# Optimization experiments

Measured on AMD Instinct MI355X. Metric: run time of the kernel, lower is better.

The kernel has to match this reference:

```python
import jax, jax.numpy as jnp
import numpy as np

N_NODES = 100000
N_EDGES = 1600000
N_FEAT = 128
N_HID = 128
N_CLS = 40
DROP_P = 0.5


def setup_inputs() -> dict:
    key = jax.random.key(0)
    k1, k2, k3, k4 = jax.random.split(key, 4)
    x = jax.random.normal(k1, (N_NODES, N_FEAT), dtype=jnp.float32)
    edge_index = jax.random.randint(k2, (2, N_EDGES), 0, N_NODES, dtype=jnp.int32)
    W1 = jax.random.normal(k3, (N_FEAT, N_HID), dtype=jnp.float32) / np.sqrt(N_FEAT)
    b1 = jnp.zeros((N_HID,), dtype=jnp.float32)
    W2 = jax.random.normal(k4, (N_HID, N_CLS), dtype=jnp.float32) / np.sqrt(N_HID)
    b2 = jnp.zeros((N_CLS,), dtype=jnp.float32)
    return {"x": x, "edge_index": edge_index, "W1": W1, "b1": b1, "W2": W2, "b2": b2}


def _gcn_norm(edge_index, num_nodes):
    # add self-loops, then symmetric normalization D^-1/2 (A+I) D^-1/2
    loops = jnp.arange(num_nodes, dtype=edge_index.dtype)
    src = jnp.concatenate([edge_index[0], loops])
    dst = jnp.concatenate([edge_index[1], loops])
    deg = jax.ops.segment_sum(jnp.ones_like(dst, dtype=jnp.float32), dst,
                              num_segments=num_nodes)
    deg_isqrt = jax.lax.rsqrt(deg)  # deg >= 1 thanks to self-loops
    norm = deg_isqrt[src] * deg_isqrt[dst]  # [E+N]
    return src, dst, norm


def _gcn_conv(x, src, dst, norm, W, b, num_nodes):
    h = x @ W                                   # [N, out]
    msg = h[src] * norm[:, None]                # gather + scale, [E+N, out]
    out = jax.ops.segment_sum(msg, dst, num_segments=num_nodes)  # scatter-add
    return out + b


def reference(x, edge_index, W1, b1, W2, b2):
    num_nodes = x.shape[0]
    src, dst, norm = _gcn_norm(edge_index, num_nodes)
    h = _gcn_conv(x, src, dst, norm, W1, b1, num_nodes)
    h = jax.nn.relu(h)
    # dropout(p=0.5, training=True) with a fixed key for determinism
    keep = jax.random.uniform(jax.random.key(42), h.shape) >= DROP_P
    h = jnp.where(keep, h / (1.0 - DROP_P), 0.0)
    out = _gcn_conv(h, src, dst, norm, W2, b2, num_nodes)
    return out
```

## Files before the change

kernel.cpp:

```cpp
#include <hip/hip_runtime.h>

#define N_NODES 100000
#define N_EDGES 1600000
#define NBUCK 196
#define G1B 3125
#define BCAP 9216

__device__ __forceinline__ unsigned pack_bf16(float a, float b){
  unsigned ua = __float_as_uint(a), ub = __float_as_uint(b);
  ua = ua + 0x7fffu + ((ua >> 16) & 1u);
  ub = ub + 0x7fffu + ((ub >> 16) & 1u);
  return (ua >> 16) | (ub & 0xffff0000u);
}
__device__ __forceinline__ unsigned short bf16_of(float a){
  unsigned ua = __float_as_uint(a);
  ua = ua + 0x7fffu + ((ua >> 16) & 1u);
  return (unsigned short)(ua >> 16);
}
__device__ __forceinline__ float bf_lo(unsigned u){ return __uint_as_float(u << 16); }
__device__ __forceinline__ float bf_hi(unsigned u){ return __uint_as_float(u & 0xffff0000u); }

__device__ __forceinline__ unsigned tf_rotl(unsigned x, int r){ return (x<<r)|(x>>(32-r)); }

__device__ __forceinline__ unsigned dropout_keep(unsigned e){
  unsigned x0 = 0u, x1 = e;
  const unsigned k0 = 0u, k1v = 42u;
  const unsigned k2 = 0x1BD11BDAu ^ k0 ^ k1v;
#define TF_R(r) { x0 += x1; x1 = tf_rotl(x1,(r)); x1 ^= x0; }
  x0 += k0; x1 += k1v;
  TF_R(13) TF_R(15) TF_R(26) TF_R(6)
  x0 += k1v; x1 += k2 + 1u;
  TF_R(17) TF_R(29) TF_R(16) TF_R(24)
  x0 += k2; x1 += k0 + 2u;
  TF_R(13) TF_R(15) TF_R(26) TF_R(6)
  x0 += k0; x1 += k1v + 3u;
  TF_R(17) TF_R(29) TF_R(16) TF_R(24)
  x0 += k1v; x1 += k2 + 4u;
  TF_R(13) TF_R(15) TF_R(26) TF_R(6)
  x0 += k2; x1 += k0 + 5u;
#undef TF_R
  return (x0 ^ x1) >> 31;
}

__device__ __forceinline__ void gemm1_block(int gb, int t, float* smem,
                                            const float* __restrict__ x,
                                            const float* __restrict__ W1,
                                            unsigned* __restrict__ h1g){
  float* xs = smem;
  float* Wq = smem + 4096;
  size_t row0 = (size_t)gb * 32;

  const float4* xv = (const float4*)(x + row0*128);
  float4* xsv = (float4*)xs;
  #pragma unroll
  for (int j = 0; j < 4; j++) xsv[t + 256*j] = xv[t + 256*j];

  int tx = t & 31, ty = t >> 5;
  float acc[4][4] = {};
  const float4* Wv = (const float4*)W1;
  float4* Wqv = (float4*)Wq;
  const float* xr = xs + (ty*4)*128;

  for (int q = 0; q < 4; q++){
    __syncthreads();
    #pragma unroll
    for (int j = 0; j < 4; j++) Wqv[t + 256*j] = Wv[q*1024 + t + 256*j];
    __syncthreads();
    int kbase = q*32;
    #pragma unroll 8
    for (int kk = 0; kk < 32; kk++){
      float4 w = *(const float4*)(Wq + kk*128 + tx*4);
      int k = kbase + kk;
      float x0 = xr[k], x1 = xr[128 + k], x2 = xr[256 + k], x3 = xr[384 + k];
      acc[0][0] = fmaf(x0, w.x, acc[0][0]); acc[0][1] = fmaf(x0, w.y, acc[0][1]);
      acc[0][2] = fmaf(x0, w.z, acc[0][2]); acc[0][3] = fmaf(x0, w.w, acc[0][3]);
      acc[1][0] = fmaf(x1, w.x, acc[1][0]); acc[1][1] = fmaf(x1, w.y, acc[1][1]);
      acc[1][2] = fmaf(x1, w.z, acc[1][2]); acc[1][3] = fmaf(x1, w.w, acc[1][3]);
      acc[2][0] = fmaf(x2, w.x, acc[2][0]); acc[2][1] = fmaf(x2, w.y, acc[2][1]);
      acc[2][2] = fmaf(x2, w.z, acc[2][2]); acc[2][3] = fmaf(x2, w.w, acc[2][3]);
      acc[3][0] = fmaf(x3, w.x, acc[3][0]); acc[3][1] = fmaf(x3, w.y, acc[3][1]);
      acc[3][2] = fmaf(x3, w.z, acc[3][2]); acc[3][3] = fmaf(x3, w.w, acc[3][3]);
    }
  }
  #pragma unroll
  for (int i = 0; i < 4; i++){
    uint2 o;
    o.x = pack_bf16(acc[i][0], acc[i][1]);
    o.y = pack_bf16(acc[i][2], acc[i][3]);
    *(uint2*)(h1g + (row0 + ty*4 + i)*64 + tx*2) = o;
  }
}

__launch_bounds__(256)
__global__ void k_B(const float* __restrict__ x, const float* __restrict__ W1,
                    unsigned* __restrict__ h1g,
                    const int* __restrict__ src, const int* __restrict__ dst,
                    int* __restrict__ bcur2,
                    int* __restrict__ tmpS, int* __restrict__ tmpD, int N, int E){
  extern __shared__ float smem[];
  int t = threadIdx.x;
  if (blockIdx.x < NBUCK){
    int* hist = (int*)smem;
    int fb = blockIdx.x;
    for (int i = t; i < NBUCK; i += 256) hist[i] = 0;
    __syncthreads();
    int e0 = fb*8192;
    #pragma unroll 4
    for (int j = 0; j < 32; j++){
      int e = e0 + t + j*256;
      if (e < E) atomicAdd(&hist[dst[e] >> 9], 1);
    }
    __syncthreads();
    if (t < NBUCK){
      int c = hist[t];
      if (c > 0) hist[t] = t*BCAP + atomicAdd(&bcur2[t], c);
    }
    __syncthreads();
    #pragma unroll 4
    for (int j = 0; j < 32; j++){
      int e = e0 + t + j*256;
      if (e < E){
        int d = dst[e], s = src[e];
        int p = atomicAdd(&hist[d >> 9], 1);
        tmpS[p] = s;
        tmpD[p] = d;
      }
    }
    return;
  }
  int gb = blockIdx.x - NBUCK;
  if (gb < G1B) gemm1_block(gb, t, smem, x, W1, h1g);
}

__launch_bounds__(512)
__global__ void k_hist(const int* __restrict__ tmpD, const int* __restrict__ bcur2,
                       int* __restrict__ degi, int* __restrict__ off,
                       float* __restrict__ dii, int N){
  __shared__ int cur[512];
  __shared__ int wtot[8];
  int b = blockIdx.x, t = threadIdx.x;
  cur[t] = 0;
  __syncthreads();
  int m = bcur2[b];
  int base = b*BCAP;
  int node0 = b << 9;
  for (int i = t; i < m; i += 512)
    atomicAdd(&cur[tmpD[base + i] - node0], 1);
  __syncthreads();
  int v = cur[t];
  int lane = t & 63, w = t >> 6;
  int incl = v;
  for (int d = 1; d < 64; d <<= 1){
    int y = __shfl_up(incl, d);
    if (lane >= d) incl += y;
  }
  if (lane == 63) wtot[w] = incl;
  __syncthreads();
  int wb = 0;
  for (int i = 0; i < w; i++) wb += wtot[i];
  int excl = wb + incl - v;
  int n = node0 + t;
  if (n < N){
    degi[n] = v;
    off[n]  = base + excl;
    dii[n]  = rsqrtf((float)(v + 1));
  }
}

__launch_bounds__(1024)
__global__ void k_csort(const int* __restrict__ tmpS, const int* __restrict__ tmpD,
                        int2* __restrict__ csre, const int* __restrict__ off,
                        const int* __restrict__ bcur2, const float* __restrict__ dii,
                        int N){
  __shared__ int   cur[512];
  __shared__ float dl[512];
  int b = blockIdx.x, t = threadIdx.x;
  int node0 = b << 9;
  if (t < 512){
    int n = node0 + t;
    cur[t] = (n < N) ? off[n] : 0;
    dl[t]  = (n < N) ? dii[n] : 0.f;
  }
  __syncthreads();
  int m = bcur2[b];
  int base = b*BCAP;
  for (int i = t; i < m; i += 1024){
    int s = tmpS[base + i];
    int d = tmpD[base + i];
    int dloc = d - node0;
    float w = dii[s] * dl[dloc];
    int p = atomicAdd(&cur[dloc], 1);
    csre[p] = make_int2(s, __float_as_int(w));
  }
}

__launch_bounds__(256)
__global__ void k_agg1(const unsigned* __restrict__ h1g, unsigned* __restrict__ Bbg,
                       const int2* __restrict__ csre, const int* __restrict__ off,
                       const int* __restrict__ degi, const float* __restrict__ dii,
                       const float* __restrict__ b1, int N){
  int n = blockIdx.x*4 + (threadIdx.x >> 6);
  int lane = threadIdx.x & 63;
  if (n >= N) return;
  n = __builtin_amdgcn_readfirstlane(n);
  float din = dii[n];
  float s2 = din*din;
  unsigned su = h1g[(size_t)n*64 + lane];
  float a0 = bf_lo(su)*s2, a1 = bf_hi(su)*s2;
  int o = off[n], cnt = degi[n];
  int i = 0;
  for (; i + 8 <= cnt; i += 8){
    int2 e0 = csre[o+i+0], e1 = csre[o+i+1], e2 = csre[o+i+2], e3 = csre[o+i+3];
    int2 e4 = csre[o+i+4], e5 = csre[o+i+5], e6 = csre[o+i+6], e7 = csre[o+i+7];
    unsigned u0 = h1g[(size_t)e0.x*64 + lane];
    unsigned u1 = h1g[(size_t)e1.x*64 + lane];
    unsigned u2 = h1g[(size_t)e2.x*64 + lane];
    unsigned u3 = h1g[(size_t)e3.x*64 + lane];
    unsigned u4 = h1g[(size_t)e4.x*64 + lane];
    unsigned u5 = h1g[(size_t)e5.x*64 + lane];
    unsigned u6 = h1g[(size_t)e6.x*64 + lane];
    unsigned u7 = h1g[(size_t)e7.x*64 + lane];
    float w0 = __int_as_float(e0.y), w1 = __int_as_float(e1.y);
    float w2 = __int_as_float(e2.y), w3 = __int_as_float(e3.y);
    float w4 = __int_as_float(e4.y), w5 = __int_as_float(e5.y);
    float w6 = __int_as_float(e6.y), w7 = __int_as_float(e7.y);
    a0 = fmaf(bf_lo(u0), w0, a0); a1 = fmaf(bf_hi(u0), w0, a1);
    a0 = fmaf(bf_lo(u1), w1, a0); a1 = fmaf(bf_hi(u1), w1, a1);
    a0 = fmaf(bf_lo(u2), w2, a0); a1 = fmaf(bf_hi(u2), w2, a1);
    a0 = fmaf(bf_lo(u3), w3, a0); a1 = fmaf(bf_hi(u3), w3, a1);
    a0 = fmaf(bf_lo(u4), w4, a0); a1 = fmaf(bf_hi(u4), w4, a1);
    a0 = fmaf(bf_lo(u5), w5, a0); a1 = fmaf(bf_hi(u5), w5, a1);
    a0 = fmaf(bf_lo(u6), w6, a0); a1 = fmaf(bf_hi(u6), w6, a1);
    a0 = fmaf(bf_lo(u7), w7, a0); a1 = fmaf(bf_hi(u7), w7, a1);
  }
  for (; i < cnt; ++i){
    int2 e = csre[o+i];
    unsigned u = h1g[(size_t)e.x*64 + lane];
    float w = __int_as_float(e.y);
    a0 = fmaf(bf_lo(u), w, a0); a1 = fmaf(bf_hi(u), w, a1);
  }
  float2 bb = *(const float2*)(b1 + lane*2);
  a0 = fmaxf(a0 + bb.x, 0.f);
  a1 = fmaxf(a1 + bb.y, 0.f);
  unsigned e0i = (unsigned)n*128u + (unsigned)lane*2u;
  a0 = dropout_keep(e0i)      ? a0*2.f : 0.f;
  a1 = dropout_keep(e0i + 1u) ? a1*2.f : 0.f;
  Bbg[(size_t)n*64 + lane] = pack_bf16(a0, a1);
}

__launch_bounds__(256)
__global__ void k_gemm2(const unsigned* __restrict__ Bbg, const float* __restrict__ W2,
                        unsigned short* __restrict__ h2g, int N){
  __shared__ float W2T[40*132];
  __shared__ float Bs[64*132];
  int t = threadIdx.x;
  int row0 = blockIdx.x * 64;
  for (int idx = t; idx < 128*40; idx += 256){
    int r = idx / 40, c = idx - 40*r;
    W2T[c*132 + r] = W2[idx];
  }
  #pragma unroll
  for (int j = 0; j < 8; j++){
    int idx = t + 256*j;
    int r = idx >> 5, c2 = idx & 31;
    int gr = row0 + r; if (gr > N-1) gr = N-1;
    uint2 v = *(const uint2*)(Bbg + (size_t)gr*64 + c2*2);
    float4 f = { bf_lo(v.x), bf_hi(v.x), bf_lo(v.y), bf_hi(v.y) };
    *(float4*)(Bs + r*132 + c2*4) = f;
  }
  __syncthreads();

  int cg = t & 7, rg = t >> 3;
  int c0 = cg*5, r0 = rg*2;
  float acc[2][5] = {};
  #pragma unroll 4
  for (int k = 0; k < 128; k++){
    float bv0 = Bs[r0*132 + k], bv1 = Bs[(r0+1)*132 + k];
    #pragma unroll
    for (int u = 0; u < 5; u++){
      float w = W2T[(c0+u)*132 + k];
      acc[0][u] = fmaf(bv0, w, acc[0][u]);
      acc[1][u] = fmaf(bv1, w, acc[1][u]);
    }
  }
  #pragma unroll
  for (int i = 0; i < 2; i++){
    int gr = row0 + r0 + i;
    if (gr < N){
      #pragma unroll
      for (int u = 0; u < 5; u++) h2g[(size_t)gr*40 + c0 + u] = bf16_of(acc[i][u]);
    }
  }
}

__launch_bounds__(256)
__global__ void k_agg2(const unsigned* __restrict__ h2u, float* __restrict__ out,
                       const int2* __restrict__ csre, const int* __restrict__ off,
                       const int* __restrict__ degi, const float* __restrict__ dii,
                       const float* __restrict__ b2, int N){
  int n = blockIdx.x*4 + (threadIdx.x >> 6);
  int lane = threadIdx.x & 63;
  if (n >= N) return;
  n = __builtin_amdgcn_readfirstlane(n);
  int g = lane / 20;
  int c = lane - 20*g;
  bool act = g < 3;
  float din = dii[n];
  float a0 = 0.f, a1 = 0.f;
  if (g == 0){
    unsigned u = h2u[(size_t)n*20 + c];
    float s2 = din*din;
    float2 bb = *(const float2*)(b2 + 2*c);
    a0 = bf_lo(u)*s2 + bb.x;
    a1 = bf_hi(u)*s2 + bb.y;
  }
  int o = off[n], cnt = degi[n];
  int i = 0;
  for (; i + 6 <= cnt; i += 6){
    int2 ea = csre[o+i+0], eb = csre[o+i+1], ec = csre[o+i+2];
    int2 ed = csre[o+i+3], ee = csre[o+i+4], ef = csre[o+i+5];
    int   sA = (g==0) ? ea.x : (g==1) ? eb.x : ec.x;
    float wA = __int_as_float((g==0) ? ea.y : (g==1) ? eb.y : ec.y);
    int   sB = (g==0) ? ed.x : (g==1) ? ee.x : ef.x;
    float wB = __int_as_float((g==0) ? ed.y : (g==1) ? ee.y : ef.y);
    unsigned uA = 0u, uB = 0u;
    if (act){
      uA = h2u[(size_t)sA*20 + c];
      uB = h2u[(size_t)sB*20 + c];
    } else { wA = 0.f; wB = 0.f; }
    a0 = fmaf(bf_lo(uA), wA, a0); a1 = fmaf(bf_hi(uA), wA, a1);
    a0 = fmaf(bf_lo(uB), wB, a0); a1 = fmaf(bf_hi(uB), wB, a1);
  }
  for (; i + 3 <= cnt; i += 3){
    int2 ea = csre[o+i+0], eb = csre[o+i+1], ec = csre[o+i+2];
    int   s = (g==0) ? ea.x : (g==1) ? eb.x : ec.x;
    float w = __int_as_float((g==0) ? ea.y : (g==1) ? eb.y : ec.y);
    unsigned u = 0u;
    if (act) u = h2u[(size_t)s*20 + c];
    else w = 0.f;
    a0 = fmaf(bf_lo(u), w, a0); a1 = fmaf(bf_hi(u), w, a1);
  }
  for (; i < cnt; ++i){
    int2 e = csre[o+i];
    if (g == 0){
      unsigned u = h2u[(size_t)e.x*20 + c];
      float w = __int_as_float(e.y);
      a0 = fmaf(bf_lo(u), w, a0); a1 = fmaf(bf_hi(u), w, a1);
    }
  }
  float t0 = __shfl(a0, (lane+20) & 63), t1 = __shfl(a1, (lane+20) & 63);
  float u0 = __shfl(a0, (lane+40) & 63), u1 = __shfl(a1, (lane+40) & 63);
  if (g == 0){
    a0 += t0 + u0; a1 += t1 + u1;
    *(float2*)(out + (size_t)n*40 + c*2) = make_float2(a0, a1);
  }
}

extern "C" void kernel_launch(void* const* d_in, const int* in_sizes, int n_in,
                              void* d_out, int out_size, void* d_ws, size_t ws_size,
                              hipStream_t stream){
  const float* x  = (const float*)d_in[0];
  const int*   ei = (const int*)  d_in[1];
  const float* W1 = (const float*)d_in[2];
  const float* b1 = (const float*)d_in[3];
  const float* W2 = (const float*)d_in[4];
  const float* b2 = (const float*)d_in[5];
  float* out = (float*)d_out;
  char* ws = (char*)d_ws;
  const int N = N_NODES, E = N_EDGES;
  const int* srcv = ei;
  const int* dstv = ei + E;

  int*   bcur2 = (int*)  (ws + 0);
  int*   off   = (int*)  (ws + 8192);
  int*   degi  = (int*)  (ws + 417792);
  float* dii   = (float*)(ws + 827392);
  int*   tmpS  = (int*)  (ws + 1236992);
  int*   tmpD  = (int*)  (ws + 8462336);
  int2*  csre  = (int2*) (ws + 15687680);
  unsigned*       h1g = (unsigned*)      (ws + 30138368);
  unsigned short* h2g = (unsigned short*)(ws + 30138368);
  unsigned*       Bbg = (unsigned*)      (ws + 55738368);

  hipMemsetAsync(bcur2, 0, 1024, stream);

  k_B<<<NBUCK + G1B, 256, 32768, stream>>>(x, W1, h1g, srcv, dstv, bcur2, tmpS, tmpD, N, E);
  k_hist<<<NBUCK, 512, 0, stream>>>(tmpD, bcur2, degi, off, dii, N);
  k_csort<<<NBUCK, 1024, 0, stream>>>(tmpS, tmpD, csre, off, bcur2, dii, N);

  k_agg1 <<<N/4, 256, 0, stream>>>(h1g, Bbg, csre, off, degi, dii, b1, N);
  k_gemm2<<<(N + 63)/64, 256, 0, stream>>>(Bbg, W2, h2g, N);
  k_agg2 <<<N/4, 256, 0, stream>>>((const unsigned*)h2g, out, csre, off, degi, dii, b2, N);
}
```

Baseline: 239.4 us.

## Pad layer-2 features to 128-byte rows and pack the bucket temporaries

k_gemm2 now writes h2 with a 64-element row stride, so each row is a 128-byte-aligned line. k_agg2 is rewritten so that each 32-lane half reads one padded row per edge, with an 8-way unrolled gather in place of the 3-group split and the cross-lane shuffle reduction. The bucket-fill stage packs src/dst into a single int2 temporary and uses more, smaller edge chunks (4096 edges per block). The aim is to cut partial-line gathers and lane-selection overhead in aggregation, at the cost of more bytes per gathered row and redundant work in the upper half-wave.

```diff
diff --git a/kernel.cpp b/kernel.cpp
--- a/kernel.cpp
+++ b/kernel.cpp
@@ -4,6 +4,8 @@
 #define N_EDGES 1600000
 #define NBUCK 196
 #define G1B 3125
+#define FB 391
+#define FEDGE 4096
 #define BCAP 9216
 
 __device__ __forceinline__ unsigned pack_bf16(float a, float b){
@@ -95,18 +97,17 @@
 __global__ void k_B(const float* __restrict__ x, const float* __restrict__ W1,
                     unsigned* __restrict__ h1g,
                     const int* __restrict__ src, const int* __restrict__ dst,
-                    int* __restrict__ bcur2,
-                    int* __restrict__ tmpS, int* __restrict__ tmpD, int N, int E){
+                    int* __restrict__ bcur2, int2* __restrict__ tmp, int N, int E){
   extern __shared__ float smem[];
   int t = threadIdx.x;
-  if (blockIdx.x < NBUCK){
+  if (blockIdx.x < FB){
     int* hist = (int*)smem;
     int fb = blockIdx.x;
     for (int i = t; i < NBUCK; i += 256) hist[i] = 0;
     __syncthreads();
-    int e0 = fb*8192;
+    int e0 = fb*FEDGE;
     #pragma unroll 4
-    for (int j = 0; j < 32; j++){
+    for (int j = 0; j < FEDGE/256; j++){
       int e = e0 + t + j*256;
       if (e < E) atomicAdd(&hist[dst[e] >> 9], 1);
     }
@@ -117,23 +118,22 @@
     }
     __syncthreads();
     #pragma unroll 4
-    for (int j = 0; j < 32; j++){
+    for (int j = 0; j < FEDGE/256; j++){
       int e = e0 + t + j*256;
       if (e < E){
         int d = dst[e], s = src[e];
         int p = atomicAdd(&hist[d >> 9], 1);
-        tmpS[p] = s;
-        tmpD[p] = d;
+        tmp[p] = make_int2(s, d);
       }
     }
     return;
   }
-  int gb = blockIdx.x - NBUCK;
+  int gb = blockIdx.x - FB;
   if (gb < G1B) gemm1_block(gb, t, smem, x, W1, h1g);
 }
 
 __launch_bounds__(512)
-__global__ void k_hist(const int* __restrict__ tmpD, const int* __restrict__ bcur2,
+__global__ void k_hist(const int2* __restrict__ tmp, const int* __restrict__ bcur2,
                        int* __restrict__ degi, int* __restrict__ off,
                        float* __restrict__ dii, int N){
   __shared__ int cur[512];
@@ -145,7 +145,7 @@
   int base = b*BCAP;
   int node0 = b << 9;
   for (int i = t; i < m; i += 512)
-    atomicAdd(&cur[tmpD[base + i] - node0], 1);
+    atomicAdd(&cur[tmp[base + i].y - node0], 1);
   __syncthreads();
   int v = cur[t];
   int lane = t & 63, w = t >> 6;
@@ -168,10 +168,9 @@
 }
 
 __launch_bounds__(1024)
-__global__ void k_csort(const int* __restrict__ tmpS, const int* __restrict__ tmpD,
-                        int2* __restrict__ csre, const int* __restrict__ off,
-                        const int* __restrict__ bcur2, const float* __restrict__ dii,
-                        int N){
+__global__ void k_csort(const int2* __restrict__ tmp, int2* __restrict__ csre,
+                        const int* __restrict__ off, const int* __restrict__ bcur2,
+                        const float* __restrict__ dii, int N){
   __shared__ int   cur[512];
   __shared__ float dl[512];
   int b = blockIdx.x, t = threadIdx.x;
@@ -185,12 +184,11 @@
   int m = bcur2[b];
   int base = b*BCAP;
   for (int i = t; i < m; i += 1024){
-    int s = tmpS[base + i];
-    int d = tmpD[base + i];
-    int dloc = d - node0;
-    float w = dii[s] * dl[dloc];
+    int2 r = tmp[base + i];
+    int dloc = r.y - node0;
+    float w = dii[r.x] * dl[dloc];
     int p = atomicAdd(&cur[dloc], 1);
-    csre[p] = make_int2(s, __float_as_int(w));
+    csre[p] = make_int2(r.x, __float_as_int(w));
   }
 }
 
@@ -250,7 +248,7 @@
 
 __launch_bounds__(256)
 __global__ void k_gemm2(const unsigned* __restrict__ Bbg, const float* __restrict__ W2,
-                        unsigned short* __restrict__ h2g, int N){
+                        unsigned short* __restrict__ h2p, int N){
   __shared__ float W2T[40*132];
   __shared__ float Bs[64*132];
   int t = threadIdx.x;
@@ -288,71 +286,62 @@
     int gr = row0 + r0 + i;
     if (gr < N){
       #pragma unroll
-      for (int u = 0; u < 5; u++) h2g[(size_t)gr*40 + c0 + u] = bf16_of(acc[i][u]);
+      for (int u = 0; u < 5; u++) h2p[(size_t)gr*64 + c0 + u] = bf16_of(acc[i][u]);
     }
   }
 }
 
 __launch_bounds__(256)
-__global__ void k_agg2(const unsigned* __restrict__ h2u, float* __restrict__ out,
+__global__ void k_agg2(const unsigned* __restrict__ h2p, float* __restrict__ out,
                        const int2* __restrict__ csre, const int* __restrict__ off,
                        const int* __restrict__ degi, const float* __restrict__ dii,
                        const float* __restrict__ b2, int N){
   int n = blockIdx.x*4 + (threadIdx.x >> 6);
-  int lane = threadIdx.x & 63;
+  int lane31 = threadIdx.x & 31;
+  int lane   = threadIdx.x & 63;
   if (n >= N) return;
   n = __builtin_amdgcn_readfirstlane(n);
-  int g = lane / 20;
-  int c = lane - 20*g;
-  bool act = g < 3;
   float din = dii[n];
-  float a0 = 0.f, a1 = 0.f;
-  if (g == 0){
-    unsigned u = h2u[(size_t)n*20 + c];
-    float s2 = din*din;
-    float2 bb = *(const float2*)(b2 + 2*c);
-    a0 = bf_lo(u)*s2 + bb.x;
-    a1 = bf_hi(u)*s2 + bb.y;
-  }
+  float s2 = din*din;
+  unsigned su = h2p[(size_t)n*32 + lane31];
+  float a0 = bf_lo(su)*s2, a1 = bf_hi(su)*s2;
   int o = off[n], cnt = degi[n];
   int i = 0;
-  for (; i + 6 <= cnt; i += 6){
-    int2 ea = csre[o+i+0], eb = csre[o+i+1], ec = csre[o+i+2];
-    int2 ed = csre[o+i+3], ee = csre[o+i+4], ef = csre[o+i+5];
-    int   sA = (g==0) ? ea.x : (g==1) ? eb.x : ec.x;
-    float wA = __int_as_float((g==0) ? ea.y : (g==1) ? eb.y : ec.y);
-    int   sB = (g==0) ? ed.x : (g==1) ? ee.x : ef.x;
-    float wB = __int_as_float((g==0) ? ed.y : (g==1) ? ee.y : ef.y);
-    unsigned uA = 0u, uB = 0u;
-    if (act){
-      uA = h2u[(size_t)sA*20 + c];
-      uB = h2u[(size_t)sB*20 + c];
-    } else { wA = 0.f; wB = 0.f; }
-    a0 = fmaf(bf_lo(uA), wA, a0); a1 = fmaf(bf_hi(uA), wA, a1);
-    a0 = fmaf(bf_lo(uB), wB, a0); a1 = fmaf(bf_hi(uB), wB, a1);
-  }
-  for (; i + 3 <= cnt; i += 3){
-    int2 ea = csre[o+i+0], eb = csre[o+i+1], ec = csre[o+i+2];
-    int   s = (g==0) ? ea.x : (g==1) ? eb.x : ec.x;
-    float w = __int_as_float((g==0) ? ea.y : (g==1) ? eb.y : ec.y);
-    unsigned u = 0u;
-    if (act) u = h2u[(size_t)s*20 + c];
-    else w = 0.f;
-    a0 = fmaf(bf_lo(u), w, a0); a1 = fmaf(bf_hi(u), w, a1);
+  for (; i + 8 <= cnt; i += 8){
+    int2 e0 = csre[o+i+0], e1 = csre[o+i+1], e2 = csre[o+i+2], e3 = csre[o+i+3];
+    int2 e4 = csre[o+i+4], e5 = csre[o+i+5], e6 = csre[o+i+6], e7 = csre[o+i+7];
+    unsigned u0 = h2p[(size_t)e0.x*32 + lane31];
+    unsigned u1 = h2p[(size_t)e1.x*32 + lane31];
+    unsigned u2 = h2p[(size_t)e2.x*32 + lane31];
+    unsigned u3 = h2p[(size_t)e3.x*32 + lane31];
+    unsigned u4 = h2p[(size_t)e4.x*32 + lane31];
+    unsigned u5 = h2p[(size_t)e5.x*32 + lane31];
+    unsigned u6 = h2p[(size_t)e6.x*32 + lane31];
+    unsigned u7 = h2p[(size_t)e7.x*32 + lane31];
+    float w0 = __int_as_float(e0.y), w1 = __int_as_float(e1.y);
+    float w2 = __int_as_float(e2.y), w3 = __int_as_float(e3.y);
+    float w4 = __int_as_float(e4.y), w5 = __int_as_float(e5.y);
+    float w6 = __int_as_float(e6.y), w7 = __int_as_float(e7.y);
+    a0 = fmaf(bf_lo(u0), w0, a0); a1 = fmaf(bf_hi(u0), w0, a1);
+    a0 = fmaf(bf_lo(u1), w1, a0); a1 = fmaf(bf_hi(u1), w1, a1);
+    a0 = fmaf(bf_lo(u2), w2, a0); a1 = fmaf(bf_hi(u2), w2, a1);
+    a0 = fmaf(bf_lo(u3), w3, a0); a1 = fmaf(bf_hi(u3), w3, a1);
+    a0 = fmaf(bf_lo(u4), w4, a0); a1 = fmaf(bf_hi(u4), w4, a1);
+    a0 = fmaf(bf_lo(u5), w5, a0); a1 = fmaf(bf_hi(u5), w5, a1);
+    a0 = fmaf(bf_lo(u6), w6, a0); a1 = fmaf(bf_hi(u6), w6, a1);
+    a0 = fmaf(bf_lo(u7), w7, a0); a1 = fmaf(bf_hi(u7), w7, a1);
   }
   for (; i < cnt; ++i){
     int2 e = csre[o+i];
-    if (g == 0){
-      unsigned u = h2u[(size_t)e.x*20 + c];
-      float w = __int_as_float(e.y);
-      a0 = fmaf(bf_lo(u), w, a0); a1 = fmaf(bf_hi(u), w, a1);
-    }
-  }
-  float t0 = __shfl(a0, (lane+20) & 63), t1 = __shfl(a1, (lane+20) & 63);
-  float u0 = __shfl(a0, (lane+40) & 63), u1 = __shfl(a1, (lane+40) & 63);
-  if (g == 0){
-    a0 += t0 + u0; a1 += t1 + u1;
-    *(float2*)(out + (size_t)n*40 + c*2) = make_float2(a0, a1);
+    unsigned u = h2p[(size_t)e.x*32 + lane31];
+    float w = __int_as_float(e.y);
+    a0 = fmaf(bf_lo(u), w, a0); a1 = fmaf(bf_hi(u), w, a1);
+  }
+  if (lane < 20){
+    float2 bb = *(const float2*)(b2 + lane*2);
+    a0 += bb.x;
+    a1 += bb.y;
+    *(float2*)(out + (size_t)n*40 + lane*2) = make_float2(a0, a1);
   }
 }
 
@@ -375,20 +364,19 @@
   int*   off   = (int*)  (ws + 8192);
   int*   degi  = (int*)  (ws + 417792);
   float* dii   = (float*)(ws + 827392);
-  int*   tmpS  = (int*)  (ws + 1236992);
-  int*   tmpD  = (int*)  (ws + 8462336);
+  int2*  tmp   = (int2*) (ws + 1236992);
   int2*  csre  = (int2*) (ws + 15687680);
   unsigned*       h1g = (unsigned*)      (ws + 30138368);
-  unsigned short* h2g = (unsigned short*)(ws + 30138368);
+  unsigned short* h2p = (unsigned short*)(ws + 30138368);
   unsigned*       Bbg = (unsigned*)      (ws + 55738368);
 
-  hipMemsetAsync(bcur2, 0, 1024, stream);
-
-  k_B<<<NBUCK + G1B, 256, 32768, stream>>>(x, W1, h1g, srcv, dstv, bcur2, tmpS, tmpD, N, E);
-  k_hist<<<NBUCK, 512, 0, stream>>>(tmpD, bcur2, degi, off, dii, N);
-  k_csort<<<NBUCK, 1024, 0, stream>>>(tmpS, tmpD, csre, off, bcur2, dii, N);
+  hipMemsetAsync(bcur2, 0, 8192, stream);
+
+  k_B<<<FB + G1B, 256, 32768, stream>>>(x, W1, h1g, srcv, dstv, bcur2, tmp, N, E);
+  k_hist<<<NBUCK, 512, 0, stream>>>(tmp, bcur2, degi, off, dii, N);
+  k_csort<<<NBUCK, 1024, 0, stream>>>(tmp, csre, off, bcur2, dii, N);
 
   k_agg1 <<<N/4, 256, 0, stream>>>(h1g, Bbg, csre, off, degi, dii, b1, N);
-  k_gemm2<<<(N + 63)/64, 256, 0, stream>>>(Bbg, W2, h2g, N);
-  k_agg2 <<<N/4, 256, 0, stream>>>((const unsigned*)h2g, out, csre, off, degi, dii, b2, N);
-}
+  k_gemm2<<<(N + 63)/64, 256, 0, stream>>>(Bbg, W2, h2p, N);
+  k_agg2 <<<N/4, 256, 0, stream>>>((const unsigned*)h2p, out, csre, off, degi, dii, b2, N);
+}
```

Measured after the change: 242.2 us. No clear change (+1.2%).
